# Optimization experiments

Measured on AMD Instinct MI355X. Metric: run time of the kernel, lower is better.

The kernel has to match this reference:

```python
import jax, jax.numpy as jnp
import numpy as np

B, N, F_IN, F_OUT = 16, 4096, 64, 64


def setup_inputs() -> dict:
    key = jax.random.key(0)
    k1, k2, k3, k4 = jax.random.split(key, 4)
    stdv = 1.0 / np.sqrt(F_OUT)
    graph = jax.random.normal(k1, (B, N, F_IN), dtype=jnp.float32)
    adj = jax.random.uniform(k2, (N, N), dtype=jnp.float32)
    weight = jax.random.uniform(k3, (F_IN, F_OUT), minval=-stdv, maxval=stdv, dtype=jnp.float32)
    bias = jax.random.uniform(k4, (F_OUT,), minval=-stdv, maxval=stdv, dtype=jnp.float32)
    return {"graph": graph, "adj": adj, "weight": weight, "bias": bias}


def _normalize_adj(adj):
    # Symmetric normalization D^{-1/2} A D^{-1/2}.
    # diag_embed @ adj @ diag_embed == row/col elementwise scaling (same math, O(N^2)).
    rowsum = jnp.sum(adj, axis=-1)
    rowsum = rowsum + (rowsum == 0).astype(adj.dtype)  # avoid div-by-zero for isolated nodes
    d_inv_sqrt = rowsum ** -0.5
    return d_inv_sqrt[:, None] * adj * d_inv_sqrt[None, :]


def reference(graph, adj, weight, bias):
    adj_norm = _normalize_adj(adj)                      # [N, N]
    support = jnp.einsum('bni,io->bno', graph, weight)  # [B, N, F_out]
    output = jnp.einsum('nm,bmo->bno', adj_norm, support)
    output = jax.nn.relu(output + bias)
    return (output, adj)
```

## Files before the change

### kernel.cpp

```cpp
#include <hip/hip_runtime.h>
#include <hip/hip_bf16.h>
#include <stdint.h>


typedef __bf16 bf16;
typedef __bf16 bf16x8 __attribute__((ext_vector_type(8)));
typedef float f32x4 __attribute__((ext_vector_type(4)));

#define NN 4096
#define BATCH 16
#define FD 64
#define CDIM 1024

__device__ __forceinline__ int swz(int q) {
    return (q & ~3) | ((q & 3) ^ ((q >> 3) & 3));
}

__global__ __launch_bounds__(256) void k_prep(const float* __restrict__ adj,
                                              bf16* __restrict__ adjb,
                                              float* __restrict__ dsq,
                                              float4* __restrict__ out1,
                                              int do_copy) {
    int row = blockIdx.x;
    const float4* p = (const float4*)(adj + (size_t)row * NN);
    uint4* q = (uint4*)(adjb + (size_t)row * NN);
    float4* o = out1 + (size_t)row * (NN / 4);
    float s = 0.f;
    for (int j = threadIdx.x; j < 512; j += 256) {
        float4 a = p[2 * j], b = p[2 * j + 1];
        if (do_copy) { o[2 * j] = a; o[2 * j + 1] = b; }
        bf16x8 h;
        h[0] = (bf16)a.x; h[1] = (bf16)a.y; h[2] = (bf16)a.z; h[3] = (bf16)a.w;
        h[4] = (bf16)b.x; h[5] = (bf16)b.y; h[6] = (bf16)b.z; h[7] = (bf16)b.w;
        q[j] = __builtin_bit_cast(uint4, h);
        s += a.x + a.y + a.z + a.w + b.x + b.y + b.z + b.w;
    }
    #pragma unroll
    for (int off = 32; off > 0; off >>= 1) s += __shfl_down(s, off, 64);
    __shared__ float red[4];
    int lane = threadIdx.x & 63, wv = threadIdx.x >> 6;
    if (lane == 0) red[wv] = s;
    __syncthreads();
    if (threadIdx.x == 0) {
        float t = red[0] + red[1] + red[2] + red[3];
        if (t == 0.f) t = 1.f;
        dsq[row] = 1.0f / sqrtf(t);
    }
}

__global__ __launch_bounds__(256) void k_support(const float* __restrict__ graph,
                                                 const float* __restrict__ weight,
                                                 const float* __restrict__ dsq,
                                                 bf16* __restrict__ spT) {
    __shared__ float wT[64 * 64];
    int tid = threadIdx.x;
    for (int idx = tid; idx < 4096; idx += 256) {
        int i = idx >> 6, o = idx & 63;
        wT[o * 64 + i] = weight[idx];
    }
    __syncthreads();
    int b = blockIdx.y;
    int m = blockIdx.x * 256 + tid;
    const float4* g4 = (const float4*)(graph + ((size_t)b * NN + m) * FD);
    float ds = dsq[m];
    float gr[64];
    #pragma unroll
    for (int j = 0; j < 16; j++) {
        float4 v = g4[j];
        gr[4 * j] = v.x * ds; gr[4 * j + 1] = v.y * ds;
        gr[4 * j + 2] = v.z * ds; gr[4 * j + 3] = v.w * ds;
    }
    bf16* outp = spT + m;
    for (int o = 0; o < 64; o++) {
        const float4* w4 = (const float4*)&wT[o * 64];
        float acc = 0.f;
        #pragma unroll
        for (int j = 0; j < 16; j++) {
            float4 wv = w4[j];
            acc += gr[4 * j] * wv.x + gr[4 * j + 1] * wv.y
                 + gr[4 * j + 2] * wv.z + gr[4 * j + 3] * wv.w;
        }
        outp[(size_t)(b * 64 + o) * NN] = (bf16)acc;
    }
}

__global__ __launch_bounds__(256, 4) void k_gemm(const bf16* __restrict__ adjb,
                                                 const bf16* __restrict__ spT,
                                                 const float* __restrict__ dsq,
                                                 float* __restrict__ part,
                                                 int kchunk) {
    __shared__ uint4 lds_a[2][512];
    __shared__ uint4 lds_b[2][512];
    const int tid = threadIdx.x;
    const int lane = tid & 63;
    const int w = tid >> 6;
    const int n0 = blockIdx.x * 128;
    const int c0 = blockIdx.y * 128;
    const size_t kbase = (size_t)blockIdx.z * kchunk;
    const int niter = kchunk >> 5;
    float* __restrict__ pp = part + (size_t)blockIdx.z * NN * CDIM;

    const int q0 = tid, q1 = tid + 256;
    const int w0 = swz(q0), w1 = swz(q1);
    const uint4* pA0 = (const uint4*)(adjb + (size_t)(n0 + (q0 >> 2)) * NN + kbase) + (q0 & 3);
    const uint4* pA1 = (const uint4*)(adjb + (size_t)(n0 + (q1 >> 2)) * NN + kbase) + (q1 & 3);
    const uint4* pB0 = (const uint4*)(spT  + (size_t)(c0 + (q0 >> 2)) * NN + kbase) + (q0 & 3);
    const uint4* pB1 = (const uint4*)(spT  + (size_t)(c0 + (q1 >> 2)) * NN + kbase) + (q1 & 3);

    const int r = lane & 15, qo = lane >> 4;
    const int rm = (w >> 1) * 64, rc = (w & 1) * 64;
    const bf16x8* fA = (const bf16x8*)&lds_a[0][0] + (rm + r) * 4 + (qo ^ (((rm + r) >> 1) & 3));
    const bf16x8* fB = (const bf16x8*)&lds_b[0][0] + (rc + r) * 4 + (qo ^ (((rc + r) >> 1) & 3));

    f32x4 ac[4][4];
    #pragma unroll
    for (int i = 0; i < 4; i++)
        #pragma unroll
        for (int j = 0; j < 4; j++)
            ac[i][j] = (f32x4){0.f, 0.f, 0.f, 0.f};

    uint4 va0 = pA0[0], va1 = pA1[0], vb0 = pB0[0], vb1 = pB1[0];
    lds_a[0][w0] = va0; lds_a[0][w1] = va1;
    lds_b[0][w0] = vb0; lds_b[0][w1] = vb1;
    if (niter > 1) { va0 = pA0[4]; va1 = pA1[4]; vb0 = pB0[4]; vb1 = pB1[4]; }
    __syncthreads();

    for (int kt = 0; kt < niter; kt++) {
        const int cur = kt & 1, nxt = cur ^ 1;
        bf16x8 af[4], bfr[4];
        const bf16x8* fAc = fA + (cur << 9);
        const bf16x8* fBc = fB + (cur << 9);
        #pragma unroll
        for (int mi = 0; mi < 4; mi++) af[mi] = fAc[mi * 64];
        #pragma unroll
        for (int ni = 0; ni < 4; ni++) bfr[ni] = fBc[ni * 64];
        if (kt + 1 < niter) {
            lds_a[nxt][w0] = va0; lds_a[nxt][w1] = va1;
            lds_b[nxt][w0] = vb0; lds_b[nxt][w1] = vb1;
            if (kt + 2 < niter) {
                const int kd = (kt + 2) * 4;
                va0 = pA0[kd]; va1 = pA1[kd]; vb0 = pB0[kd]; vb1 = pB1[kd];
            }
        }
        __syncthreads();
        #pragma unroll
        for (int mi = 0; mi < 4; mi++)
            #pragma unroll
            for (int ni = 0; ni < 4; ni++)
                ac[mi][ni] = __builtin_amdgcn_mfma_f32_16x16x32_bf16(
                    af[mi], bfr[ni], ac[mi][ni], 0, 0, 0);
    }

    #pragma unroll
    for (int mi = 0; mi < 4; mi++) {
        float dn[4];
        #pragma unroll
        for (int rr = 0; rr < 4; rr++) dn[rr] = dsq[n0 + rm + mi * 16 + qo * 4 + rr];
        #pragma unroll
        for (int ni = 0; ni < 4; ni++) {
            int c = c0 + rc + ni * 16 + r;
            #pragma unroll
            for (int rr = 0; rr < 4; rr++) {
                int n = n0 + rm + mi * 16 + qo * 4 + rr;
                pp[(size_t)n * CDIM + c] = dn[rr] * ac[mi][ni][rr];
            }
        }
    }
}

__global__ __launch_bounds__(256) void k_epi(const float4* __restrict__ part,
                                             int nsplit,
                                             const float* __restrict__ bias,
                                             float4* __restrict__ out0) {
    int idx = blockIdx.x * 256 + threadIdx.x;
    int flat = idx * 4;
    int o4 = flat & 63;
    int n = (flat >> 6) & (NN - 1);
    int b = flat >> 18;
    size_t off = ((size_t)n * CDIM + b * 64 + o4) >> 2;
    const size_t zstride = (size_t)NN * CDIM / 4;
    float4 a = part[off];
    for (int z = 1; z < nsplit; z++) {
        float4 t = part[off + z * zstride];
        a.x += t.x; a.y += t.y; a.z += t.z; a.w += t.w;
    }
    float4 bv = *(const float4*)(bias + o4);
    float4 r;
    r.x = fmaxf(a.x + bv.x, 0.f);
    r.y = fmaxf(a.y + bv.y, 0.f);
    r.z = fmaxf(a.z + bv.z, 0.f);
    r.w = fmaxf(a.w + bv.w, 0.f);
    out0[idx] = r;
}

__global__ __launch_bounds__(256) void k_copy(const float4* __restrict__ src,
                                              float4* __restrict__ dst) {
    size_t i = (size_t)blockIdx.x * 256 + threadIdx.x;
    dst[i] = src[i];
}

extern "C" void kernel_launch(void* const* d_in, const int* in_sizes, int n_in,
                              void* d_out, int out_size, void* d_ws, size_t ws_size,
                              hipStream_t stream) {
    const float *graph = nullptr, *adj = nullptr, *weight = nullptr, *bias = nullptr;
    for (int i = 0; i < n_in; i++) {
        const float* p = (const float*)d_in[i];
        switch (in_sizes[i]) {
            case BATCH * NN * FD: graph  = p; break;
            case NN * NN:         adj    = p; break;
            case FD * FD:         weight = p; break;
            case FD:              bias   = p; break;
        }
    }

    float* out0 = (float*)d_out;
    float* out1 = out0 + (size_t)BATCH * NN * FD;

    const size_t SZ_ADJB = (size_t)NN * NN * 2;
    const size_t SZ_SPT  = (size_t)CDIM * NN * 2;
    const size_t SZ_DSQ  = (size_t)NN * 4;
    const size_t SZ_PART = (size_t)NN * CDIM * 4;

    bf16 *adjb, *spT; float *dsq, *part;
    int nsplit, do_copy_in_prep;
    if (ws_size >= SZ_ADJB + SZ_SPT + SZ_DSQ + 4 * SZ_PART) {
        nsplit = 4; do_copy_in_prep = 1;
        char* s = (char*)d_ws;
        adjb = (bf16*)s;
        spT  = (bf16*)(s + SZ_ADJB);
        dsq  = (float*)(s + SZ_ADJB + SZ_SPT);
        part = (float*)(s + SZ_ADJB + SZ_SPT + SZ_DSQ);
    } else if (ws_size >= SZ_ADJB + SZ_SPT + SZ_DSQ + 2 * SZ_PART) {
        nsplit = 2; do_copy_in_prep = 1;
        char* s = (char*)d_ws;
        adjb = (bf16*)s;
        spT  = (bf16*)(s + SZ_ADJB);
        dsq  = (float*)(s + SZ_ADJB + SZ_SPT);
        part = (float*)(s + SZ_ADJB + SZ_SPT + SZ_DSQ);
    } else {
        nsplit = 2; do_copy_in_prep = 0;
        part = (float*)out1;
        adjb = (bf16*)((char*)out1 + 2 * SZ_PART);
        spT  = (bf16*)out0;
        dsq  = (float*)((char*)out0 + SZ_SPT);
    }
    const int kchunk = NN / nsplit;

    hipLaunchKernelGGL(k_prep, dim3(NN), dim3(256), 0, stream,
                       adj, adjb, dsq, (float4*)out1, do_copy_in_prep);
    hipLaunchKernelGGL(k_support, dim3(16, 16), dim3(256), 0, stream,
                       graph, weight, dsq, spT);
    hipLaunchKernelGGL(k_gemm, dim3(32, 8, nsplit), dim3(256), 0, stream,
                       adjb, spT, dsq, part, kchunk);
    hipLaunchKernelGGL(k_epi, dim3(4096), dim3(256), 0, stream,
                       (const float4*)part, nsplit, bias, (float4*)out0);
    if (!do_copy_in_prep) {
        hipLaunchKernelGGL(k_copy, dim3(16384), dim3(256), 0, stream,
                           (const float4*)adj, (float4*)out1);
    }
}
```

Baseline: 243.3 us.

## Use direct global-to-LDS loads in GEMM and store split-K partials as bf16

The GEMM's register-staged double buffer is replaced with global_load_lds direct copies into a single LDS buffer, fenced by two barriers per k-step. Split-K partial sums are now written and read as bf16 instead of fp32, halving partial-buffer traffic between the GEMM and the epilogue. The fallback workspace path moves to four splits. In exchange, loads no longer overlap compute within a block and the partials lose precision.

```diff
diff --git a/kernel.cpp b/kernel.cpp
--- a/kernel.cpp
+++ b/kernel.cpp
@@ -4,6 +4,7 @@
 
 
 typedef __bf16 bf16;
+typedef __bf16 bf16x4 __attribute__((ext_vector_type(4)));
 typedef __bf16 bf16x8 __attribute__((ext_vector_type(8)));
 typedef float f32x4 __attribute__((ext_vector_type(4)));
 
@@ -11,10 +12,6 @@
 #define BATCH 16
 #define FD 64
 #define CDIM 1024
-
-__device__ __forceinline__ int swz(int q) {
-    return (q & ~3) | ((q & 3) ^ ((q >> 3) & 3));
-}
 
 __global__ __launch_bounds__(256) void k_prep(const float* __restrict__ adj,
                                               bf16* __restrict__ adjb,
@@ -87,10 +84,10 @@
 __global__ __launch_bounds__(256, 4) void k_gemm(const bf16* __restrict__ adjb,
                                                  const bf16* __restrict__ spT,
                                                  const float* __restrict__ dsq,
-                                                 float* __restrict__ part,
+                                                 bf16* __restrict__ part,
                                                  int kchunk) {
-    __shared__ uint4 lds_a[2][512];
-    __shared__ uint4 lds_b[2][512];
+    __shared__ bf16x8 lds_a[512];
+    __shared__ bf16x8 lds_b[512];
     const int tid = threadIdx.x;
     const int lane = tid & 63;
     const int w = tid >> 6;
@@ -98,19 +95,25 @@
     const int c0 = blockIdx.y * 128;
     const size_t kbase = (size_t)blockIdx.z * kchunk;
     const int niter = kchunk >> 5;
-    float* __restrict__ pp = part + (size_t)blockIdx.z * NN * CDIM;
-
-    const int q0 = tid, q1 = tid + 256;
-    const int w0 = swz(q0), w1 = swz(q1);
-    const uint4* pA0 = (const uint4*)(adjb + (size_t)(n0 + (q0 >> 2)) * NN + kbase) + (q0 & 3);
-    const uint4* pA1 = (const uint4*)(adjb + (size_t)(n0 + (q1 >> 2)) * NN + kbase) + (q1 & 3);
-    const uint4* pB0 = (const uint4*)(spT  + (size_t)(c0 + (q0 >> 2)) * NN + kbase) + (q0 & 3);
-    const uint4* pB1 = (const uint4*)(spT  + (size_t)(c0 + (q1 >> 2)) * NN + kbase) + (q1 & 3);
+    bf16* __restrict__ pp = part + (size_t)blockIdx.z * NN * CDIM;
+
+    const bf16* gA[2]; const bf16* gB[2];
+    bf16x8* lA[2]; bf16x8* lB[2];
+    #pragma unroll
+    for (int j = 0; j < 2; j++) {
+        int g = (w * 2 + j) * 64 + lane;
+        int row = g >> 2;
+        int sub = (g & 3) ^ ((g >> 3) & 3);
+        gA[j] = adjb + (size_t)(n0 + row) * NN + kbase + sub * 8;
+        gB[j] = spT  + (size_t)(c0 + row) * NN + kbase + sub * 8;
+        lA[j] = &lds_a[(w * 2 + j) * 64];
+        lB[j] = &lds_b[(w * 2 + j) * 64];
+    }
 
     const int r = lane & 15, qo = lane >> 4;
     const int rm = (w >> 1) * 64, rc = (w & 1) * 64;
-    const bf16x8* fA = (const bf16x8*)&lds_a[0][0] + (rm + r) * 4 + (qo ^ (((rm + r) >> 1) & 3));
-    const bf16x8* fB = (const bf16x8*)&lds_b[0][0] + (rc + r) * 4 + (qo ^ (((rc + r) >> 1) & 3));
+    const bf16x8* fA = lds_a + (rm + r) * 4 + (qo ^ (((rm + r) >> 1) & 3));
+    const bf16x8* fB = lds_b + (rc + r) * 4 + (qo ^ (((rc + r) >> 1) & 3));
 
     f32x4 ac[4][4];
     #pragma unroll
@@ -119,30 +122,24 @@
         for (int j = 0; j < 4; j++)
             ac[i][j] = (f32x4){0.f, 0.f, 0.f, 0.f};
 
-    uint4 va0 = pA0[0], va1 = pA1[0], vb0 = pB0[0], vb1 = pB1[0];
-    lds_a[0][w0] = va0; lds_a[0][w1] = va1;
-    lds_b[0][w0] = vb0; lds_b[0][w1] = vb1;
-    if (niter > 1) { va0 = pA0[4]; va1 = pA1[4]; vb0 = pB0[4]; vb1 = pB1[4]; }
-    __syncthreads();
-
-    for (int kt = 0; kt < niter; kt++) {
-        const int cur = kt & 1, nxt = cur ^ 1;
+    for (int it = 0; it < niter; it++) {
+        const int kt = it * 32;
+        __syncthreads();
+        #pragma unroll
+        for (int j = 0; j < 2; j++) {
+            __builtin_amdgcn_global_load_lds(
+                (const __attribute__((address_space(1))) void*)(gA[j] + kt),
+                (__attribute__((address_space(3))) void*)lA[j], 16, 0, 0);
+            __builtin_amdgcn_global_load_lds(
+                (const __attribute__((address_space(1))) void*)(gB[j] + kt),
+                (__attribute__((address_space(3))) void*)lB[j], 16, 0, 0);
+        }
+        __syncthreads();
         bf16x8 af[4], bfr[4];
-        const bf16x8* fAc = fA + (cur << 9);
-        const bf16x8* fBc = fB + (cur << 9);
-        #pragma unroll
-        for (int mi = 0; mi < 4; mi++) af[mi] = fAc[mi * 64];
-        #pragma unroll
-        for (int ni = 0; ni < 4; ni++) bfr[ni] = fBc[ni * 64];
-        if (kt + 1 < niter) {
-            lds_a[nxt][w0] = va0; lds_a[nxt][w1] = va1;
-            lds_b[nxt][w0] = vb0; lds_b[nxt][w1] = vb1;
-            if (kt + 2 < niter) {
-                const int kd = (kt + 2) * 4;
-                va0 = pA0[kd]; va1 = pA1[kd]; vb0 = pB0[kd]; vb1 = pB1[kd];
-            }
-        }
-        __syncthreads();
+        #pragma unroll
+        for (int mi = 0; mi < 4; mi++) af[mi] = fA[mi * 64];
+        #pragma unroll
+        for (int ni = 0; ni < 4; ni++) bfr[ni] = fB[ni * 64];
         #pragma unroll
         for (int mi = 0; mi < 4; mi++)
             #pragma unroll
@@ -162,13 +159,13 @@
             #pragma unroll
             for (int rr = 0; rr < 4; rr++) {
                 int n = n0 + rm + mi * 16 + qo * 4 + rr;
-                pp[(size_t)n * CDIM + c] = dn[rr] * ac[mi][ni][rr];
+                pp[(size_t)n * CDIM + c] = (bf16)(dn[rr] * ac[mi][ni][rr]);
             }
         }
     }
 }
 
-__global__ __launch_bounds__(256) void k_epi(const float4* __restrict__ part,
+__global__ __launch_bounds__(256) void k_epi(const bf16* __restrict__ part,
                                              int nsplit,
                                              const float* __restrict__ bias,
                                              float4* __restrict__ out0) {
@@ -177,19 +174,19 @@
     int o4 = flat & 63;
     int n = (flat >> 6) & (NN - 1);
     int b = flat >> 18;
-    size_t off = ((size_t)n * CDIM + b * 64 + o4) >> 2;
-    const size_t zstride = (size_t)NN * CDIM / 4;
-    float4 a = part[off];
-    for (int z = 1; z < nsplit; z++) {
-        float4 t = part[off + z * zstride];
-        a.x += t.x; a.y += t.y; a.z += t.z; a.w += t.w;
+    size_t off = (size_t)n * CDIM + b * 64 + o4;
+    const size_t zstride = (size_t)NN * CDIM;
+    float ax = 0.f, ay = 0.f, az = 0.f, aw = 0.f;
+    for (int z = 0; z < nsplit; z++) {
+        bf16x4 t = *(const bf16x4*)(part + off + z * zstride);
+        ax += (float)t[0]; ay += (float)t[1]; az += (float)t[2]; aw += (float)t[3];
     }
     float4 bv = *(const float4*)(bias + o4);
     float4 r;
-    r.x = fmaxf(a.x + bv.x, 0.f);
-    r.y = fmaxf(a.y + bv.y, 0.f);
-    r.z = fmaxf(a.z + bv.z, 0.f);
-    r.w = fmaxf(a.w + bv.w, 0.f);
+    r.x = fmaxf(ax + bv.x, 0.f);
+    r.y = fmaxf(ay + bv.y, 0.f);
+    r.z = fmaxf(az + bv.z, 0.f);
+    r.w = fmaxf(aw + bv.w, 0.f);
     out0[idx] = r;
 }
 
@@ -219,9 +216,9 @@
     const size_t SZ_ADJB = (size_t)NN * NN * 2;
     const size_t SZ_SPT  = (size_t)CDIM * NN * 2;
     const size_t SZ_DSQ  = (size_t)NN * 4;
-    const size_t SZ_PART = (size_t)NN * CDIM * 4;
-
-    bf16 *adjb, *spT; float *dsq, *part;
+    const size_t SZ_PART = (size_t)NN * CDIM * 2;
+
+    bf16 *adjb, *spT, *part; float *dsq;
     int nsplit, do_copy_in_prep;
     if (ws_size >= SZ_ADJB + SZ_SPT + SZ_DSQ + 4 * SZ_PART) {
         nsplit = 4; do_copy_in_prep = 1;
@@ -229,18 +226,18 @@
         adjb = (bf16*)s;
         spT  = (bf16*)(s + SZ_ADJB);
         dsq  = (float*)(s + SZ_ADJB + SZ_SPT);
-        part = (float*)(s + SZ_ADJB + SZ_SPT + SZ_DSQ);
+        part = (bf16*)(s + SZ_ADJB + SZ_SPT + SZ_DSQ);
     } else if (ws_size >= SZ_ADJB + SZ_SPT + SZ_DSQ + 2 * SZ_PART) {
         nsplit = 2; do_copy_in_prep = 1;
         char* s = (char*)d_ws;
         adjb = (bf16*)s;
         spT  = (bf16*)(s + SZ_ADJB);
         dsq  = (float*)(s + SZ_ADJB + SZ_SPT);
-        part = (float*)(s + SZ_ADJB + SZ_SPT + SZ_DSQ);
+        part = (bf16*)(s + SZ_ADJB + SZ_SPT + SZ_DSQ);
     } else {
-        nsplit = 2; do_copy_in_prep = 0;
-        part = (float*)out1;
-        adjb = (bf16*)((char*)out1 + 2 * SZ_PART);
+        nsplit = 4; do_copy_in_prep = 0;
+        part = (bf16*)out1;
+        adjb = (bf16*)((char*)out1 + 4 * SZ_PART);
         spT  = (bf16*)out0;
         dsq  = (float*)((char*)out0 + SZ_SPT);
     }
@@ -253,7 +250,7 @@
     hipLaunchKernelGGL(k_gemm, dim3(32, 8, nsplit), dim3(256), 0, stream,
                        adjb, spT, dsq, part, kchunk);
     hipLaunchKernelGGL(k_epi, dim3(4096), dim3(256), 0, stream,
-                       (const float4*)part, nsplit, bias, (float4*)out0);
+                       part, nsplit, bias, (float4*)out0);
     if (!do_copy_in_prep) {
         hipLaunchKernelGGL(k_copy, dim3(16384), dim3(256), 0, stream,
                            (const float4*)adj, (float4*)out1);
```

After: 234.7 us. 1.04x faster.
